# Kernel optimization log

Measured on AMD Instinct MI355X. Metric: run time of the kernel, lower is better.

Reference implementation:

```python
import jax, jax.numpy as jnp
from jax import lax
import numpy as np

K_IN, K_OUT, H, ML = 32, 16, 256, 80
L_PRE, L_FWD, B = 60, 80, 1024


def gru_cell(x, h, Wih, Whh, bih, bhh):
    # torch GRU gate order: r, z, n
    gi = x @ Wih.T + bih
    gh = h @ Whh.T + bhh
    ir, iz, inn = jnp.split(gi, 3, axis=-1)
    hr, hz, hn = jnp.split(gh, 3, axis=-1)
    r = jax.nn.sigmoid(ir + hr)
    z = jax.nn.sigmoid(iz + hz)
    n = jnp.tanh(inn + r * hn)
    return (1.0 - z) * n + z * h


def setup_inputs() -> dict:
    key = jax.random.key(0)
    ks = jax.random.split(key, 24)
    s = 0.05
    rn = lambda k, shp: (jax.random.normal(k, shp) * s).astype(jnp.float32)
    inp = {
        "pre_x": jax.random.normal(ks[0], (L_PRE, B, K_IN), dtype=jnp.float32),
        "pre_y": jax.random.normal(ks[1], (L_PRE, B, K_OUT), dtype=jnp.float32),
        "forward_x": jax.random.normal(ks[2], (L_FWD, B, K_IN), dtype=jnp.float32),
        # encoder: embedding Linear(k_in+k_out -> H), GRU(H,H)
        "enc_emb_W": rn(ks[3], (H, K_IN + K_OUT)),
        "enc_emb_b": rn(ks[4], (H,)),
        "enc_Wih": rn(ks[5], (3 * H, H)),
        "enc_Whh": rn(ks[6], (3 * H, H)),
        "enc_bih": rn(ks[7], (3 * H,)),
        "enc_bhh": rn(ks[8], (3 * H,)),
        # decoder: embedding Linear(k_out+k_in -> H), attn Linear(2H -> ML),
        # attn_combine Linear(2H -> H), GRU(H,H), out Linear(H -> k_out)
        "dec_emb_W": rn(ks[9], (H, K_OUT + K_IN)),
        "dec_emb_b": rn(ks[10], (H,)),
        "attn_W": rn(ks[11], (ML, 2 * H)),
        "attn_b": rn(ks[12], (ML,)),
        "comb_W": rn(ks[13], (H, 2 * H)),
        "comb_b": rn(ks[14], (H,)),
        "dec_Wih": rn(ks[15], (3 * H, H)),
        "dec_Whh": rn(ks[16], (3 * H, H)),
        "dec_bih": rn(ks[17], (3 * H,)),
        "dec_bhh": rn(ks[18], (3 * H,)),
        "out_W": rn(ks[19], (K_OUT, H)),
        "out_b": rn(ks[20], (K_OUT,)),
    }
    return inp


def reference(pre_x, pre_y, forward_x,
              enc_emb_W, enc_emb_b, enc_Wih, enc_Whh, enc_bih, enc_bhh,
              dec_emb_W, dec_emb_b, attn_W, attn_b, comb_W, comb_b,
              dec_Wih, dec_Whh, dec_bih, dec_bhh, out_W, out_b):
    L_pre, batch, _ = pre_x.shape
    hdim = enc_emb_b.shape[0]
    max_len = attn_b.shape[0]

    # ---- encoder ----
    emb = jnp.concatenate([pre_x, pre_y], axis=2) @ enc_emb_W.T + enc_emb_b  # [L_pre,B,H]
    h0 = jnp.zeros((batch, hdim), dtype=pre_x.dtype)

    def enc_step(h, x):
        h2 = gru_cell(x, h, enc_Wih, enc_Whh, enc_bih, enc_bhh)
        return h2, h2

    enc_h, enc_outs = lax.scan(enc_step, h0, emb)
    # pad encoder outputs to max_length along time (zeros beyond L_pre)
    enc_outputs = jnp.zeros((max_len, batch, hdim), dtype=pre_x.dtype).at[:L_pre].set(enc_outs)
    enc_bmh = enc_outputs.transpose(1, 0, 2)  # [B, ML, H]

    # ---- decoder (dropout inactive: eval mode) ----
    def dec_step(carry, fx):
        y, h = carry
        di = jnp.concatenate([y, fx], axis=-1)            # [B, k_out+k_in]
        e = di @ dec_emb_W.T + dec_emb_b                   # [B, H]
        logits = jnp.concatenate([e, h], axis=-1) @ attn_W.T + attn_b  # [B, ML]
        aw = jax.nn.softmax(logits, axis=-1)
        ctx = jnp.einsum('bm,bmh->bh', aw, enc_bmh)        # [B, H]
        g = jnp.tanh(jnp.concatenate([e, ctx], axis=-1) @ comb_W.T + comb_b)
        h2 = gru_cell(g, h, dec_Wih, dec_Whh, dec_bih, dec_bhh)
        y2 = h2 @ out_W.T + out_b                          # [B, k_out]
        return (y2, h2), y2

    y_init = jnp.zeros_like(pre_y[0])
    _, ys = lax.scan(dec_step, (y_init, enc_h), forward_x)
    return ys  # [L_fwd, B, k_out]
```

## Files before the change

### kernel.cpp

```cpp
#include <hip/hip_runtime.h>
#include <hip/hip_bf16.h>

#define BATCH 1024
#define HD 256
#define MLEN 80
#define LPRE 60
#define LFWD 80
#define KIN 32
#define KOUT 16

typedef unsigned short bf16_t;
typedef __attribute__((ext_vector_type(8))) short bf16x8;
typedef __attribute__((ext_vector_type(4))) float f32x4;
typedef __attribute__((ext_vector_type(4))) unsigned u32x4;

#define MFMA __builtin_amdgcn_mfma_f32_16x16x32_bf16

__device__ __forceinline__ float bf2f(bf16_t v){ return __uint_as_float(((unsigned)v)<<16); }
__device__ __forceinline__ bf16_t f2bf(float f){
    unsigned u = __float_as_uint(f);
    return (bf16_t)((u + 0x7FFFu + ((u>>16)&1u)) >> 16);
}
__device__ __forceinline__ unsigned pack2(float lo, float hi){
    return (unsigned)f2bf(lo) | ((unsigned)f2bf(hi)<<16);
}
__device__ __forceinline__ float bflo(unsigned d){ return __uint_as_float(d<<16); }
__device__ __forceinline__ float bfhi(unsigned d){ return __uint_as_float(d & 0xffff0000u); }
__device__ __forceinline__ float sigm(float x){ return 1.0f/(1.0f+__expf(-x)); }

#define OFF_Z  262144
#define OFF_IN 524288
#define OFF_HN 655360

__global__ void pack_gru(const float* __restrict__ Wih, const float* __restrict__ Whh,
                         bf16_t* __restrict__ dst)
{
    int T = blockIdx.x*256 + threadIdx.x;
    int grp, local;
    if (T < 16384){ grp=0; local=T; }
    else if (T < 32768){ grp=1; local=T-16384; }
    else if (T < 40960){ grp=2; local=T-32768; }
    else { grp=3; local=T-40960; }
    int nkt = (grp<2)?16:8;
    int nt  = local / (nkt*64);
    int rem = local - nt*(nkt*64);
    int kt  = rem >> 6;
    int l   = rem & 63;
    int n   = nt*16 + (l&15);
    int k0  = kt*32 + ((l>>4)<<3);
    unsigned w[4];
    #pragma unroll
    for (int h2=0; h2<4; h2++){
        float v[2];
        #pragma unroll
        for (int s=0; s<2; s++){
            int k = k0 + h2*2 + s;
            if (grp==0)      v[s] = (k<256)? Wih[(size_t)n*HD + k]       : Whh[(size_t)n*HD + (k-256)];
            else if (grp==1) v[s] = (k<256)? Wih[(size_t)(256+n)*HD + k] : Whh[(size_t)(256+n)*HD + (k-256)];
            else if (grp==2) v[s] = Wih[(size_t)(512+n)*HD + k];
            else             v[s] = Whh[(size_t)(512+n)*HD + k];
        }
        w[h2] = pack2(v[0], v[1]);
    }
    uint4 u = {w[0],w[1],w[2],w[3]};
    *(uint4*)((char*)dst + (size_t)T*16) = u;
}

__global__ void pack_B512(const float* __restrict__ W, bf16_t* __restrict__ dst)
{
    int T = blockIdx.x*256 + threadIdx.x;
    int nt = T >> 10, kt = (T>>6)&15, l = T&63;
    int n = nt*16 + (l&15);
    int k0 = kt*32 + ((l>>4)<<3);
    unsigned w[4];
    #pragma unroll
    for (int h2=0; h2<4; h2++)
        w[h2] = pack2(W[(size_t)n*512 + k0+h2*2], W[(size_t)n*512 + k0+h2*2+1]);
    uint4 u = {w[0],w[1],w[2],w[3]};
    *(uint4*)((char*)dst + (size_t)T*16) = u;
}

__global__ void wfuse_kernel(const float* __restrict__ dembW, const float* __restrict__ dembB,
                             const float* __restrict__ outW, const float* __restrict__ outB,
                             float* __restrict__ Wfuse, float* __restrict__ ebias)
{
    int T = blockIdx.x*256 + threadIdx.x;
    if (T < 65536){
        int k = T >> 8, n = T & 255;
        float acc = 0.f;
        #pragma unroll
        for (int o=0;o<16;o++) acc += dembW[(size_t)n*48 + o]*outW[(size_t)o*HD + k];
        Wfuse[(size_t)k*HD + n] = acc;
    } else if (T < 65792){
        int n = T - 65536;
        float acc = dembB[n];
        #pragma unroll
        for (int o=0;o<16;o++) acc += outB[o]*dembW[(size_t)n*48 + o];
        ebias[n] = acc;
    }
}

__global__ void pack_logits(const float* __restrict__ Wfuse, const float* __restrict__ dembW,
                            const float* __restrict__ attW, const float* __restrict__ attB,
                            const float* __restrict__ dembB, const float* __restrict__ ebias,
                            bf16_t* __restrict__ BL, bf16_t* __restrict__ BL0,
                            float* __restrict__ lb, float* __restrict__ lb0)
{
    int T = blockIdx.x*256 + threadIdx.x;
    if (T < 5760){
        int variant = (T < 2880) ? 0 : 1;
        int local = variant ? (T-2880) : T;
        int nt = local/576, rem = local - nt*576;
        int kt = rem >> 6, l = rem & 63;
        int m  = nt*16 + (l&15);
        int k0 = kt*32 + ((l>>4)<<3);
        unsigned w[4];
        #pragma unroll
        for (int h2=0; h2<4; h2++){
            float v[2];
            for (int s=0;s<2;s++){
                int k = k0 + h2*2 + s;
                float acc;
                if (kt < 8){
                    if (variant == 0){
                        acc = attW[(size_t)m*512 + 256 + k];
                        for (int n=0;n<256;n++) acc += Wfuse[(size_t)k*HD + n]*attW[(size_t)m*512 + n];
                    } else {
                        acc = attW[(size_t)m*512 + 256 + k];
                    }
                } else {
                    int kp = k - 256;
                    acc = 0.f;
                    for (int n=0;n<256;n++) acc += dembW[(size_t)n*48 + 16 + kp]*attW[(size_t)m*512 + n];
                }
                v[s] = acc;
            }
            w[h2] = pack2(v[0], v[1]);
        }
        uint4 u = {w[0],w[1],w[2],w[3]};
        bf16_t* d = variant ? BL0 : BL;
        *(uint4*)((char*)d + (size_t)local*16) = u;
    } else if (T < 5840){
        int m = T - 5760;
        float acc = attB[m];
        for (int n=0;n<256;n++) acc += ebias[n]*attW[(size_t)m*512 + n];
        lb[m] = acc;
    } else if (T < 5920){
        int m = T - 5840;
        float acc = attB[m];
        for (int n=0;n<256;n++) acc += dembB[n]*attW[(size_t)m*512 + n];
        lb0[m] = acc;
    }
}

__global__ void pack_gfold(const float* __restrict__ Wfuse, const float* __restrict__ dembW,
                           const float* __restrict__ combW, const float* __restrict__ combB,
                           const float* __restrict__ ebias, const float* __restrict__ dembB,
                           bf16_t* __restrict__ dst, float* __restrict__ cbf, float* __restrict__ cbf0)
{
    int T = blockIdx.x*256 + threadIdx.x;
    if (T < 9216){
        int nt = T/576, rem = T - nt*576;
        int kt = rem >> 6, l = rem & 63;
        int n = nt*16 + (l&15);
        int k0 = kt*32 + ((l>>4)<<3);
        unsigned w[4];
        for (int h2=0; h2<4; h2++){
            float v[2];
            for (int s=0;s<2;s++){
                int k = k0 + h2*2 + s;
                float acc = 0.f;
                if (k < 256){
                    for (int j=0;j<256;j++) acc += Wfuse[(size_t)k*HD + j]*combW[(size_t)n*512 + j];
                } else {
                    int kp = k - 256;
                    for (int j=0;j<256;j++) acc += dembW[(size_t)j*48 + 16 + kp]*combW[(size_t)n*512 + j];
                }
                v[s] = acc;
            }
            w[h2] = pack2(v[0], v[1]);
        }
        uint4 u = {w[0],w[1],w[2],w[3]};
        *(uint4*)((char*)dst + (size_t)T*16) = u;
    } else if (T < 9472){
        int n = T - 9216;
        float acc = combB[n];
        for (int j=0;j<256;j++) acc += ebias[j]*combW[(size_t)n*512 + j];
        cbf[n] = acc;
    } else if (T < 9728){
        int n = T - 9472;
        float acc = combB[n];
        for (int j=0;j<256;j++) acc += dembB[j]*combW[(size_t)n*512 + j];
        cbf0[n] = acc;
    }
}

__global__ void pack_out(const float* __restrict__ outW, bf16_t* __restrict__ dst)
{
    int T = blockIdx.x*256 + threadIdx.x;
    int kt = T >> 6, l = T & 63;
    int n  = l & 15;
    int k0 = kt*32 + ((l>>4)<<3);
    unsigned w[4];
    #pragma unroll
    for (int h2=0; h2<4; h2++)
        w[h2] = pack2(outW[(size_t)n*HD + k0+h2*2], outW[(size_t)n*HD + k0+h2*2+1]);
    uint4 u = {w[0],w[1],w[2],w[3]};
    *(uint4*)((char*)dst + (size_t)T*16) = u;
}

__global__ __launch_bounds__(256) void emb_kernel(
    const float* __restrict__ px, const float* __restrict__ py,
    const float* __restrict__ embW, const float* __restrict__ embB,
    bf16_t* __restrict__ emb)
{
    __shared__ float Ws[256*49];
    __shared__ float xy[16][48];
    __shared__ float bs[256];
    int t = blockIdx.y, b0 = blockIdx.x*16, tid = threadIdx.x;
    for (int i = tid; i < 256*48; i += 256){ int n=i/48, k=i-n*48; Ws[n*49+k]=embW[i]; }
    bs[tid] = embB[tid];
    for (int i = tid; i < 16*48; i += 256){
        int r=i/48, k=i-r*48;
        xy[r][k] = (k<KIN)? px[((size_t)t*BATCH + b0+r)*KIN + k]
                          : py[((size_t)t*BATCH + b0+r)*KOUT + (k-KIN)];
    }
    __syncthreads();
    int n = tid;
    const float* w = &Ws[n*49];
    for (int r=0;r<16;r++){
        float acc = bs[n];
        #pragma unroll
        for (int k=0;k<48;k++) acc += xy[r][k]*w[k];
        emb[((size_t)t*BATCH + b0+r)*HD + n] = f2bf(acc);
    }
}

__global__ void fxconv(const float* __restrict__ fx, bf16_t* __restrict__ dst)
{
    size_t i = (size_t)blockIdx.x*256 + threadIdx.x;
    const float4* s = (const float4*)(fx + i*8);
    float4 a = s[0], b = s[1];
    uint4 u = { pack2(a.x,a.y), pack2(a.z,a.w), pack2(b.x,b.y), pack2(b.z,b.w) };
    *(uint4*)(dst + i*8) = u;
}

__global__ __launch_bounds__(256) void pgemm(
    const bf16_t* __restrict__ enc, const bf16_t* __restrict__ Bcmb,
    bf16_t* __restrict__ P)
{
    __shared__ __align__(16) bf16_t As[16][264];
    __shared__ __align__(16) bf16_t Gs[16][264];
    int tid = threadIdx.x, b0 = blockIdx.x*16, t = blockIdx.y;
    const bf16_t* src = enc + ((size_t)t*BATCH + b0)*HD;
    for (int i = tid; i < 512; i += 256){
        int r = i>>5, c = i&31;
        *(uint4*)&As[r][c*8] = *(const uint4*)(src + (size_t)r*HD + c*8);
    }
    __syncthreads();
    int lane = tid&63, wave = tid>>6;
    const bf16_t* arow = &As[lane&15][(lane>>4)*8];
    size_t loff = (size_t)lane*16;
    #pragma unroll
    for (int u=0; u<4; u++){
        int nt = wave*4 + u;
        f32x4 c = {0,0,0,0};
        #pragma unroll
        for (int k8=0; k8<8; k8++){
            bf16x8 a = *(const bf16x8*)(arow + k8*32);
            bf16x8 b = *(const bf16x8*)((const char*)Bcmb + (size_t)(((nt<<4)+8+k8)<<10) + loff);
            c = MFMA(a, b, c, 0,0,0);
        }
        int n = (nt<<4) + (lane&15);
        #pragma unroll
        for (int q=0;q<4;q++) Gs[((lane>>4)<<2)+q][n] = f2bf(c[q]);
    }
    __syncthreads();
    bf16_t* dst = P + ((size_t)t*BATCH + b0)*HD;
    for (int i = tid; i < 512; i += 256){
        int r = i>>5, c = i&31;
        *(uint4*)(dst + (size_t)r*HD + c*8) = *(const uint4*)&Gs[r][c*8];
    }
}

__global__ __launch_bounds__(512) void gru_step2(
    const bf16_t* __restrict__ A0, const bf16_t* __restrict__ A1,
    const bf16_t* __restrict__ Bp,
    const float* __restrict__ bih, const float* __restrict__ bhh,
    const float* __restrict__ hprev, float* __restrict__ hnext,
    bf16_t* __restrict__ hnext_bf, bf16_t* __restrict__ extra_bf)
{
    __shared__ __align__(16) bf16_t As[16][520];
    __shared__ __align__(16) f32x4 redR[4][64];
    __shared__ __align__(16) f32x4 redZ[4][64];
    __shared__ __align__(16) f32x4 redI[4][64];
    int tid = threadIdx.x, b0 = blockIdx.x*16;
    for (int i = tid; i < 1024; i += 512){
        int r = i>>6, c = i&63;
        const bf16_t* src = (c<32)? (A0 + (size_t)(b0+r)*HD + c*8)
                                  : (A1 + (size_t)(b0+r)*HD + (c-32)*8);
        *(uint4*)&As[r][c*8] = *(const uint4*)src;
    }
    __syncthreads();
    int lane = tid & 63, wave = tid >> 6;
    int pairId = wave >> 1, half = wave & 1;
    int jt = blockIdx.y*4 + pairId;
    const char* arow = (const char*)&As[lane&15][(lane>>4)*8];
    const char* bpc = (const char*)Bp;
    size_t loff = (size_t)lane*16;
    size_t offX = half ? (size_t)OFF_HN : (size_t)OFF_IN;
    int kt0 = half*8;
    f32x4 cr={0,0,0,0}, cz={0,0,0,0}, cx={0,0,0,0};
    #pragma unroll
    for (int k8=0; k8<8; k8++){
        int kt = kt0 + k8;
        bf16x8 a  = *(const bf16x8*)(arow + kt*64);
        bf16x8 br = *(const bf16x8*)(bpc + (size_t)(((jt<<4)+kt)<<10) + loff);
        bf16x8 bz = *(const bf16x8*)(bpc + OFF_Z + (size_t)(((jt<<4)+kt)<<10) + loff);
        bf16x8 bx = *(const bf16x8*)(bpc + offX + (size_t)(((jt<<3)+k8)<<10) + loff);
        cr = MFMA(a, br, cr, 0,0,0);
        cz = MFMA(a, bz, cz, 0,0,0);
        cx = MFMA(a, bx, cx, 0,0,0);
    }
    if (half == 0){
        redR[pairId][lane] = cr;
        redZ[pairId][lane] = cz;
        redI[pairId][lane] = cx;
    }
    __syncthreads();
    if (half == 1){
        f32x4 crA = redR[pairId][lane];
        f32x4 czA = redZ[pairId][lane];
        f32x4 ci  = redI[pairId][lane];
        int j = (jt<<4) + (lane&15);
        float b_r = bih[j] + bhh[j];
        float b_z = bih[256+j] + bhh[256+j];
        float b_i = bih[512+j], b_h = bhh[512+j];
        #pragma unroll
        for (int q=0;q<4;q++){
            int b = b0 + ((lane>>4)<<2) + q;
            float rv = sigm(cr[q] + crA[q] + b_r);
            float zv = sigm(cz[q] + czA[q] + b_z);
            float nv = tanhf(ci[q] + b_i + rv*(cx[q] + b_h));
            float h2 = (1.0f - zv)*nv + zv*hprev[(size_t)b*HD + j];
            hnext[(size_t)b*HD + j] = h2;
            bf16_t hb = f2bf(h2);
            hnext_bf[(size_t)b*HD + j] = hb;
            extra_bf[(size_t)b*HD + j] = hb;
        }
    }
}

__global__ __launch_bounds__(512) void dec_attn(
    const bf16_t* __restrict__ hbf, const bf16_t* __restrict__ fxt,
    const bf16_t* __restrict__ BL, const bf16_t* __restrict__ Bout,
    const float* __restrict__ lbp, const float* __restrict__ outB,
    int t, float* __restrict__ aw, float* __restrict__ out)
{
    __shared__ __align__(16) bf16_t As[16][296];
    __shared__ float awL[16][84];
    int tid = threadIdx.x, b0 = blockIdx.x*16;
    for (int i = tid; i < 576; i += 512){
        int r = i/36, c = i - r*36;
        const bf16_t* src = (c<32)? (hbf + (size_t)(b0+r)*HD + c*8)
                                  : (fxt + (size_t)(b0+r)*KIN + (c-32)*8);
        *(uint4*)&As[r][c*8] = *(const uint4*)src;
    }
    __syncthreads();
    int lane = tid & 63, wave = tid >> 6;
    const bf16_t* arow = &As[lane&15][(lane>>4)*8];
    size_t loff = (size_t)lane*16;
    if (wave < 5){
        f32x4 c = {0,0,0,0};
        #pragma unroll
        for (int kt = 0; kt < 9; kt++){
            bf16x8 a = *(const bf16x8*)(arow + kt*32);
            bf16x8 b = *(const bf16x8*)((const char*)BL + (size_t)((wave*9+kt)<<10) + loff);
            c = MFMA(a, b, c, 0,0,0);
        }
        int m = (wave<<4) + (lane&15);
        float bbm = lbp[m];
        #pragma unroll
        for (int q=0;q<4;q++) awL[((lane>>4)<<2)+q][m] = c[q] + bbm;
    } else if (wave == 5 && t > 0){
        f32x4 c = {0,0,0,0};
        #pragma unroll
        for (int kt = 0; kt < 8; kt++){
            bf16x8 a = *(const bf16x8*)(arow + kt*32);
            bf16x8 b = *(const bf16x8*)((const char*)Bout + (size_t)(kt<<10) + loff);
            c = MFMA(a, b, c, 0,0,0);
        }
        int o = lane & 15;
        float bo = outB[o];
        #pragma unroll
        for (int q=0;q<4;q++){
            int r = ((lane>>4)<<2) + q;
            out[((size_t)(t-1)*BATCH + b0+r)*KOUT + o] = c[q] + bo;
        }
    }
    __syncthreads();
    if (tid < 256){
        int r2 = tid >> 4, l2 = tid & 15;
        float vmax = -1e30f;
        for (int m=l2; m<80; m+=16) vmax = fmaxf(vmax, awL[r2][m]);
        #pragma unroll
        for (int k=1; k<16; k<<=1) vmax = fmaxf(vmax, __shfl_xor(vmax, k, 16));
        float ps = 0.f;
        for (int m=l2; m<80; m+=16){ float v = __expf(awL[r2][m]-vmax); awL[r2][m]=v; ps += v; }
        #pragma unroll
        for (int k=1; k<16; k<<=1) ps += __shfl_xor(ps, k, 16);
        float inv = 1.0f/ps;
        for (int m=l2; m<80; m+=16) aw[(size_t)(b0+r2)*80 + m] = awL[r2][m]*inv;
    }
}

__global__ __launch_bounds__(256) void dec_gcomb(
    const bf16_t* __restrict__ hbf, const bf16_t* __restrict__ fxt,
    const float* __restrict__ aw, const bf16_t* __restrict__ P,
    const bf16_t* __restrict__ Bgf, const float* __restrict__ cbf,
    int kt0, bf16_t* __restrict__ g_out)
{
    __shared__ __align__(16) bf16_t As[16][296];
    __shared__ float aws[16][80];
    __shared__ float pre[16][68];
    __shared__ float part[2][16][64];
    int tid = threadIdx.x, b0 = blockIdx.x*16, y = blockIdx.y;

    int half = tid >> 7;
    int u = tid & 127;
    int r_ = u >> 3;
    int c8 = u & 7;
    const bf16_t* pbp = P + ((size_t)(half*30)*BATCH + (b0+r_))*HD + y*64 + c8*8;
    u32x4 pf[15];
    #pragma unroll
    for (int i=0;i<15;i++) pf[i] = *(const u32x4*)(pbp + (size_t)i*BATCH*HD);

    for (int i = tid; i < 576; i += 256){
        int r = i/36, c = i - r*36;
        const bf16_t* src = (c<32)? (hbf + (size_t)(b0+r)*HD + c*8)
                                  : (fxt + (size_t)(b0+r)*KIN + (c-32)*8);
        *(uint4*)&As[r][c*8] = *(const uint4*)src;
    }
    for (int i = tid; i < 1280; i += 256){
        int r = i/80, m = i - r*80;
        aws[r][m] = aw[(size_t)(b0+r)*80 + m];
    }
    __syncthreads();

    int lane = tid & 63, wave = tid >> 6;
    {
        const bf16_t* arow = &As[lane&15][(lane>>4)*8];
        size_t loff = (size_t)lane*16;
        int nt = y*4 + wave;
        f32x4 c = {0,0,0,0};
        for (int kt=kt0; kt<9; kt++){
            bf16x8 a = *(const bf16x8*)(arow + kt*32);
            bf16x8 b = *(const bf16x8*)((const char*)Bgf + (size_t)((nt*9+kt)<<10) + loff);
            c = MFMA(a, b, c, 0,0,0);
        }
        #pragma unroll
        for (int q=0;q<4;q++) pre[((lane>>4)<<2)+q][wave*16 + (lane&15)] = c[q];
    }

    float acc[8];
    #pragma unroll
    for (int i=0;i<8;i++) acc[i]=0.f;
    const float* awr = &aws[r_][half*30];
    #pragma unroll
    for (int i=0;i<15;i++){
        float w = awr[i];
        acc[0]=fmaf(w,bflo(pf[i][0]),acc[0]); acc[1]=fmaf(w,bfhi(pf[i][0]),acc[1]);
        acc[2]=fmaf(w,bflo(pf[i][1]),acc[2]); acc[3]=fmaf(w,bfhi(pf[i][1]),acc[3]);
        acc[4]=fmaf(w,bflo(pf[i][2]),acc[4]); acc[5]=fmaf(w,bfhi(pf[i][2]),acc[5]);
        acc[6]=fmaf(w,bflo(pf[i][3]),acc[6]); acc[7]=fmaf(w,bfhi(pf[i][3]),acc[7]);
    }
    #pragma unroll 5
    for (int i=15;i<30;i++){
        u32x4 v = *(const u32x4*)(pbp + (size_t)i*BATCH*HD);
        float w = awr[i];
        acc[0]=fmaf(w,bflo(v[0]),acc[0]); acc[1]=fmaf(w,bfhi(v[0]),acc[1]);
        acc[2]=fmaf(w,bflo(v[1]),acc[2]); acc[3]=fmaf(w,bfhi(v[1]),acc[3]);
        acc[4]=fmaf(w,bflo(v[2]),acc[4]); acc[5]=fmaf(w,bfhi(v[2]),acc[5]);
        acc[6]=fmaf(w,bflo(v[3]),acc[6]); acc[7]=fmaf(w,bfhi(v[3]),acc[7]);
    }
    {
        float4 p0 = {acc[0],acc[1],acc[2],acc[3]};
        float4 p1 = {acc[4],acc[5],acc[6],acc[7]};
        *(float4*)&part[half][r_][c8*8]   = p0;
        *(float4*)&part[half][r_][c8*8+4] = p1;
    }
    __syncthreads();

    if (tid < 128){
        int r = tid >> 3, cc = (tid & 7)*8;
        int n0 = y*64 + cc;
        unsigned ov[4];
        #pragma unroll
        for (int p2=0;p2<4;p2++){
            float g0 = tanhf(pre[r][cc+p2*2]   + part[0][r][cc+p2*2]   + part[1][r][cc+p2*2]   + cbf[n0+p2*2]);
            float g1 = tanhf(pre[r][cc+p2*2+1] + part[0][r][cc+p2*2+1] + part[1][r][cc+p2*2+1] + cbf[n0+p2*2+1]);
            ov[p2] = pack2(g0, g1);
        }
        uint4 uu = {ov[0],ov[1],ov[2],ov[3]};
        *(uint4*)(g_out + (size_t)(b0+r)*HD + n0) = uu;
    }
}

__global__ __launch_bounds__(256) void final79(
    const float* __restrict__ hf, const float* __restrict__ outW,
    const float* __restrict__ outB, float* __restrict__ ys)
{
    __shared__ float hs[16][260];
    __shared__ float ow[16*260];
    int tid = threadIdx.x, b0 = blockIdx.x*16;
    for (int i=tid;i<4096;i+=256){ int o2=i>>8,k=i&255; ow[o2*260+k]=outW[(size_t)o2*HD+k]; }
    for (int i=tid;i<4096;i+=256){ int r=i>>8,k=i&255; hs[r][k]=hf[(size_t)(b0+r)*HD+k]; }
    __syncthreads();
    int r=tid>>4, o=tid&15;
    float acc=outB[o];
    const float* w=&ow[o*260];
    for(int k=0;k<256;k++) acc += hs[r][k]*w[k];
    ys[((size_t)79*BATCH + b0+r)*KOUT + o] = acc;
}

extern "C" void kernel_launch(void* const* d_in, const int* in_sizes, int n_in,
                              void* d_out, int out_size, void* d_ws, size_t ws_size,
                              hipStream_t stream) {
    const float* pre_x    = (const float*)d_in[0];
    const float* pre_y    = (const float*)d_in[1];
    const float* fwd_x    = (const float*)d_in[2];
    const float* enc_embW = (const float*)d_in[3];
    const float* enc_embB = (const float*)d_in[4];
    const float* enc_Wih  = (const float*)d_in[5];
    const float* enc_Whh  = (const float*)d_in[6];
    const float* enc_bih  = (const float*)d_in[7];
    const float* enc_bhh  = (const float*)d_in[8];
    const float* dec_embW = (const float*)d_in[9];
    const float* dec_embB = (const float*)d_in[10];
    const float* attn_W   = (const float*)d_in[11];
    const float* attn_b   = (const float*)d_in[12];
    const float* comb_W   = (const float*)d_in[13];
    const float* comb_b   = (const float*)d_in[14];
    const float* dec_Wih  = (const float*)d_in[15];
    const float* dec_Whh  = (const float*)d_in[16];
    const float* dec_bih  = (const float*)d_in[17];
    const float* dec_bhh  = (const float*)d_in[18];
    const float* out_W    = (const float*)d_in[19];
    const float* out_b    = (const float*)d_in[20];
    float* out = (float*)d_out;

    char* ws = (char*)d_ws;
    size_t o = 0;
    auto alloc = [&](size_t bytes)->char*{
        char* p = ws + o; o = (o + bytes + 255) & ~(size_t)255; return p;
    };
    bf16_t* EMB     = (bf16_t*)alloc((size_t)LPRE*BATCH*HD*2);
    bf16_t* ENC_OUT = (bf16_t*)alloc((size_t)LPRE*BATCH*HD*2);
    bf16_t* PBUF    = (bf16_t*)alloc((size_t)LPRE*BATCH*HD*2);
    bf16_t* FXB     = (bf16_t*)alloc((size_t)LFWD*BATCH*KIN*2);
    float*  HF0     = (float*) alloc((size_t)BATCH*HD*4);
    float*  HF1     = (float*) alloc((size_t)BATCH*HD*4);
    bf16_t* HB0     = (bf16_t*)alloc((size_t)BATCH*HD*2);
    bf16_t* HB1     = (bf16_t*)alloc((size_t)BATCH*HD*2);
    bf16_t* GBUF    = (bf16_t*)alloc((size_t)BATCH*HD*2);
    bf16_t* DUMMY   = (bf16_t*)alloc((size_t)BATCH*HD*2);
    float*  AWB     = (float*) alloc((size_t)BATCH*80*4);
    float*  WFUSE   = (float*) alloc((size_t)256*256*4);
    float*  EBIAS   = (float*) alloc(256*4);
    float*  LB      = (float*) alloc(80*4);
    float*  LB0     = (float*) alloc(80*4);
    float*  CBF     = (float*) alloc(256*4);
    float*  CBF0    = (float*) alloc(256*4);
    bf16_t* PACK_ENC = (bf16_t*)alloc(786432);
    bf16_t* PACK_DEC = (bf16_t*)alloc(786432);
    bf16_t* PACK_CMB = (bf16_t*)alloc(262144);
    bf16_t* PACK_GF  = (bf16_t*)alloc(147456);
    bf16_t* PACK_BL  = (bf16_t*)alloc(46080);
    bf16_t* PACK_BL0 = (bf16_t*)alloc(46080);
    bf16_t* PACK_OUT = (bf16_t*)alloc(8192);

    hipMemsetAsync(HF0, 0, (size_t)BATCH*HD*4, stream);
    hipMemsetAsync(HB0, 0, (size_t)BATCH*HD*2, stream);

    dim3 blk(256);
    emb_kernel<<<dim3(64,60), blk, 0, stream>>>(pre_x, pre_y, enc_embW, enc_embB, EMB);
    fxconv<<<dim3(1280), blk, 0, stream>>>(fwd_x, FXB);
    pack_gru<<<dim3(192), blk, 0, stream>>>(enc_Wih, enc_Whh, PACK_ENC);
    pack_gru<<<dim3(192), blk, 0, stream>>>(dec_Wih, dec_Whh, PACK_DEC);
    pack_B512<<<dim3(64), blk, 0, stream>>>(comb_W, PACK_CMB);
    wfuse_kernel<<<dim3(257), blk, 0, stream>>>(dec_embW, dec_embB, out_W, out_b, WFUSE, EBIAS);
    pack_logits<<<dim3(24), blk, 0, stream>>>(WFUSE, dec_embW, attn_W, attn_b, dec_embB,
                                              EBIAS, PACK_BL, PACK_BL0, LB, LB0);
    pack_gfold<<<dim3(38), blk, 0, stream>>>(WFUSE, dec_embW, comb_W, comb_b,
                                             EBIAS, dec_embB, PACK_GF, CBF, CBF0);
    pack_out<<<dim3(2), blk, 0, stream>>>(out_W, PACK_OUT);

    float*  HF[2] = {HF0, HF1};
    bf16_t* HB[2] = {HB0, HB1};
    int p = 0;

    for (int t = 0; t < LPRE; t++){
        gru_step2<<<dim3(64,4), dim3(512), 0, stream>>>(
            EMB + (size_t)t*BATCH*HD, HB[p], PACK_ENC, enc_bih, enc_bhh,
            HF[p], HF[p^1], HB[p^1], ENC_OUT + (size_t)t*BATCH*HD);
        p ^= 1;
    }
    pgemm<<<dim3(64,60), blk, 0, stream>>>(ENC_OUT, PACK_CMB, PBUF);

    for (int t = 0; t < LFWD; t++){
        const bf16_t* fxt = FXB + (size_t)t*BATCH*KIN;
        dec_attn<<<dim3(64), dim3(512), 0, stream>>>(
            HB[p], fxt, t ? PACK_BL : PACK_BL0, PACK_OUT,
            t ? LB : LB0, out_b, t, AWB, out);
        dec_gcomb<<<dim3(64,4), blk, 0, stream>>>(
            HB[p], fxt, AWB, PBUF, PACK_GF, t ? CBF : CBF0, t ? 0 : 8, GBUF);
        gru_step2<<<dim3(64,4), dim3(512), 0, stream>>>(
            GBUF, HB[p], PACK_DEC, dec_bih, dec_bhh,
            HF[p], HF[p^1], HB[p^1], DUMMY);
        p ^= 1;
    }
    final79<<<dim3(64), blk, 0, stream>>>(HF[p], out_W, out_b, out);
}
```

Before: 2.553 ms.

## Fuse decoder attention and combine kernels into one 1024-thread block

Merges dec_attn and dec_gcomb into a single dec_front kernel, so the attention weights stay in shared memory instead of round-tripping through a global buffer, and one launch per decoder step is removed. Each block now handles all 256 hidden columns for 16 batch rows with 1024 threads, prefetching the P context rows while the attention logits are computed. The cost is fewer blocks (64 instead of 256 for the combine phase), heavier register and shared-memory use per block, and extra barriers, which may lower parallelism and latency hiding.

```diff
diff --git a/kernel.cpp b/kernel.cpp
--- a/kernel.cpp
+++ b/kernel.cpp
@@ -351,25 +351,45 @@
     }
 }
 
-__global__ __launch_bounds__(512) void dec_attn(
+__global__ __launch_bounds__(1024) void dec_front(
     const bf16_t* __restrict__ hbf, const bf16_t* __restrict__ fxt,
-    const bf16_t* __restrict__ BL, const bf16_t* __restrict__ Bout,
-    const float* __restrict__ lbp, const float* __restrict__ outB,
-    int t, float* __restrict__ aw, float* __restrict__ out)
+    const bf16_t* __restrict__ P,
+    const bf16_t* __restrict__ BL, const bf16_t* __restrict__ Bgf,
+    const bf16_t* __restrict__ Bout,
+    const float* __restrict__ lbp, const float* __restrict__ cbf,
+    const float* __restrict__ outB,
+    int t, bf16_t* __restrict__ g_out, float* __restrict__ out)
 {
     __shared__ __align__(16) bf16_t As[16][296];
     __shared__ float awL[16][84];
+    __shared__ float Cpart[16][256];
+    __shared__ float CbF[16][260];
+
     int tid = threadIdx.x, b0 = blockIdx.x*16;
-    for (int i = tid; i < 576; i += 512){
-        int r = i/36, c = i - r*36;
+
+    if (tid < 576){
+        int r = tid/36, c = tid - r*36;
         const bf16_t* src = (c<32)? (hbf + (size_t)(b0+r)*HD + c*8)
                                   : (fxt + (size_t)(b0+r)*KIN + (c-32)*8);
         *(uint4*)&As[r][c*8] = *(const uint4*)src;
     }
-    __syncthreads();
+
+    int half = tid >> 9;
+    int u    = tid & 511;
+    int cr_  = u >> 5;
+    int cc0  = (u & 31) * 8;
+    const bf16_t* cbp = P + ((size_t)(half*30)*BATCH + (b0+cr_))*HD + cc0;
+    u32x4 pf[10];
+    #pragma unroll
+    for (int i=0;i<10;i++) pf[i] = *(const u32x4*)(cbp + (size_t)i*BATCH*HD);
+
+    __syncthreads();
+
     int lane = tid & 63, wave = tid >> 6;
     const bf16_t* arow = &As[lane&15][(lane>>4)*8];
     size_t loff = (size_t)lane*16;
+    int kt0 = t ? 0 : 8;
+
     if (wave < 5){
         f32x4 c = {0,0,0,0};
         #pragma unroll
@@ -399,6 +419,7 @@
         }
     }
     __syncthreads();
+
     if (tid < 256){
         int r2 = tid >> 4, l2 = tid & 15;
         float vmax = -1e30f;
@@ -410,99 +431,65 @@
         #pragma unroll
         for (int k=1; k<16; k<<=1) ps += __shfl_xor(ps, k, 16);
         float inv = 1.0f/ps;
-        for (int m=l2; m<80; m+=16) aw[(size_t)(b0+r2)*80 + m] = awL[r2][m]*inv;
-    }
-}
-
-__global__ __launch_bounds__(256) void dec_gcomb(
-    const bf16_t* __restrict__ hbf, const bf16_t* __restrict__ fxt,
-    const float* __restrict__ aw, const bf16_t* __restrict__ P,
-    const bf16_t* __restrict__ Bgf, const float* __restrict__ cbf,
-    int kt0, bf16_t* __restrict__ g_out)
-{
-    __shared__ __align__(16) bf16_t As[16][296];
-    __shared__ float aws[16][80];
-    __shared__ float pre[16][68];
-    __shared__ float part[2][16][64];
-    int tid = threadIdx.x, b0 = blockIdx.x*16, y = blockIdx.y;
-
-    int half = tid >> 7;
-    int u = tid & 127;
-    int r_ = u >> 3;
-    int c8 = u & 7;
-    const bf16_t* pbp = P + ((size_t)(half*30)*BATCH + (b0+r_))*HD + y*64 + c8*8;
-    u32x4 pf[15];
+        for (int m=l2; m<80; m+=16) awL[r2][m] *= inv;
+    }
+    __syncthreads();
+
+    float acc[8];
     #pragma unroll
-    for (int i=0;i<15;i++) pf[i] = *(const u32x4*)(pbp + (size_t)i*BATCH*HD);
-
-    for (int i = tid; i < 576; i += 256){
-        int r = i/36, c = i - r*36;
-        const bf16_t* src = (c<32)? (hbf + (size_t)(b0+r)*HD + c*8)
-                                  : (fxt + (size_t)(b0+r)*KIN + (c-32)*8);
-        *(uint4*)&As[r][c*8] = *(const uint4*)src;
-    }
-    for (int i = tid; i < 1280; i += 256){
-        int r = i/80, m = i - r*80;
-        aws[r][m] = aw[(size_t)(b0+r)*80 + m];
-    }
-    __syncthreads();
-
-    int lane = tid & 63, wave = tid >> 6;
+    for (int i=0;i<8;i++) acc[i] = 0.f;
     {
-        const bf16_t* arow = &As[lane&15][(lane>>4)*8];
-        size_t loff = (size_t)lane*16;
-        int nt = y*4 + wave;
+        const float* awr = &awL[cr_][half*30];
+        #pragma unroll
+        for (int i=0;i<10;i++){
+            float w = awr[i];
+            acc[0]=fmaf(w,bflo(pf[i][0]),acc[0]); acc[1]=fmaf(w,bfhi(pf[i][0]),acc[1]);
+            acc[2]=fmaf(w,bflo(pf[i][1]),acc[2]); acc[3]=fmaf(w,bfhi(pf[i][1]),acc[3]);
+            acc[4]=fmaf(w,bflo(pf[i][2]),acc[4]); acc[5]=fmaf(w,bfhi(pf[i][2]),acc[5]);
+            acc[6]=fmaf(w,bflo(pf[i][3]),acc[6]); acc[7]=fmaf(w,bfhi(pf[i][3]),acc[7]);
+        }
+        #pragma unroll 5
+        for (int i=10;i<30;i++){
+            u32x4 v = *(const u32x4*)(cbp + (size_t)i*BATCH*HD);
+            float w = awr[i];
+            acc[0]=fmaf(w,bflo(v[0]),acc[0]); acc[1]=fmaf(w,bfhi(v[0]),acc[1]);
+            acc[2]=fmaf(w,bflo(v[1]),acc[2]); acc[3]=fmaf(w,bfhi(v[1]),acc[3]);
+            acc[4]=fmaf(w,bflo(v[2]),acc[4]); acc[5]=fmaf(w,bfhi(v[2]),acc[5]);
+            acc[6]=fmaf(w,bflo(v[3]),acc[6]); acc[7]=fmaf(w,bfhi(v[3]),acc[7]);
+        }
+    }
+    if (half == 0){
+        float4 p0 = {acc[0],acc[1],acc[2],acc[3]};
+        float4 p1 = {acc[4],acc[5],acc[6],acc[7]};
+        *(float4*)&Cpart[cr_][cc0]   = p0;
+        *(float4*)&Cpart[cr_][cc0+4] = p1;
+    }
+    __syncthreads();
+
+    if (half == 1){
+        float4 p0 = *(const float4*)&Cpart[cr_][cc0];
+        float4 p1 = *(const float4*)&Cpart[cr_][cc0+4];
+        float4 o0 = {acc[0]+p0.x, acc[1]+p0.y, acc[2]+p0.z, acc[3]+p0.w};
+        float4 o1 = {acc[4]+p1.x, acc[5]+p1.y, acc[6]+p1.z, acc[7]+p1.w};
+        *(float4*)&CbF[cr_][cc0]   = o0;
+        *(float4*)&CbF[cr_][cc0+4] = o1;
+    }
+    __syncthreads();
+
+    {
         f32x4 c = {0,0,0,0};
         for (int kt=kt0; kt<9; kt++){
             bf16x8 a = *(const bf16x8*)(arow + kt*32);
-            bf16x8 b = *(const bf16x8*)((const char*)Bgf + (size_t)((nt*9+kt)<<10) + loff);
+            bf16x8 b = *(const bf16x8*)((const char*)Bgf + (size_t)((wave*9+kt)<<10) + loff);
             c = MFMA(a, b, c, 0,0,0);
         }
-        #pragma unroll
-        for (int q=0;q<4;q++) pre[((lane>>4)<<2)+q][wave*16 + (lane&15)] = c[q];
-    }
-
-    float acc[8];
-    #pragma unroll
-    for (int i=0;i<8;i++) acc[i]=0.f;
-    const float* awr = &aws[r_][half*30];
-    #pragma unroll
-    for (int i=0;i<15;i++){
-        float w = awr[i];
-        acc[0]=fmaf(w,bflo(pf[i][0]),acc[0]); acc[1]=fmaf(w,bfhi(pf[i][0]),acc[1]);
-        acc[2]=fmaf(w,bflo(pf[i][1]),acc[2]); acc[3]=fmaf(w,bfhi(pf[i][1]),acc[3]);
-        acc[4]=fmaf(w,bflo(pf[i][2]),acc[4]); acc[5]=fmaf(w,bfhi(pf[i][2]),acc[5]);
-        acc[6]=fmaf(w,bflo(pf[i][3]),acc[6]); acc[7]=fmaf(w,bfhi(pf[i][3]),acc[7]);
-    }
-    #pragma unroll 5
-    for (int i=15;i<30;i++){
-        u32x4 v = *(const u32x4*)(pbp + (size_t)i*BATCH*HD);
-        float w = awr[i];
-        acc[0]=fmaf(w,bflo(v[0]),acc[0]); acc[1]=fmaf(w,bfhi(v[0]),acc[1]);
-        acc[2]=fmaf(w,bflo(v[1]),acc[2]); acc[3]=fmaf(w,bfhi(v[1]),acc[3]);
-        acc[4]=fmaf(w,bflo(v[2]),acc[4]); acc[5]=fmaf(w,bfhi(v[2]),acc[5]);
-        acc[6]=fmaf(w,bflo(v[3]),acc[6]); acc[7]=fmaf(w,bfhi(v[3]),acc[7]);
-    }
-    {
-        float4 p0 = {acc[0],acc[1],acc[2],acc[3]};
-        float4 p1 = {acc[4],acc[5],acc[6],acc[7]};
-        *(float4*)&part[half][r_][c8*8]   = p0;
-        *(float4*)&part[half][r_][c8*8+4] = p1;
-    }
-    __syncthreads();
-
-    if (tid < 128){
-        int r = tid >> 3, cc = (tid & 7)*8;
-        int n0 = y*64 + cc;
-        unsigned ov[4];
-        #pragma unroll
-        for (int p2=0;p2<4;p2++){
-            float g0 = tanhf(pre[r][cc+p2*2]   + part[0][r][cc+p2*2]   + part[1][r][cc+p2*2]   + cbf[n0+p2*2]);
-            float g1 = tanhf(pre[r][cc+p2*2+1] + part[0][r][cc+p2*2+1] + part[1][r][cc+p2*2+1] + cbf[n0+p2*2+1]);
-            ov[p2] = pack2(g0, g1);
-        }
-        uint4 uu = {ov[0],ov[1],ov[2],ov[3]};
-        *(uint4*)(g_out + (size_t)(b0+r)*HD + n0) = uu;
+        int n = (wave<<4) + (lane&15);
+        float bb = cbf[n];
+        #pragma unroll
+        for (int q=0;q<4;q++){
+            int r = ((lane>>4)<<2) + q;
+            g_out[(size_t)(b0+r)*HD + n] = f2bf(tanhf(c[q] + CbF[r][n] + bb));
+        }
     }
 }
 
@@ -564,7 +551,6 @@
     bf16_t* HB1     = (bf16_t*)alloc((size_t)BATCH*HD*2);
     bf16_t* GBUF    = (bf16_t*)alloc((size_t)BATCH*HD*2);
     bf16_t* DUMMY   = (bf16_t*)alloc((size_t)BATCH*HD*2);
-    float*  AWB     = (float*) alloc((size_t)BATCH*80*4);
     float*  WFUSE   = (float*) alloc((size_t)256*256*4);
     float*  EBIAS   = (float*) alloc(256*4);
     float*  LB      = (float*) alloc(80*4);
@@ -609,11 +595,11 @@
 
     for (int t = 0; t < LFWD; t++){
         const bf16_t* fxt = FXB + (size_t)t*BATCH*KIN;
-        dec_attn<<<dim3(64), dim3(512), 0, stream>>>(
-            HB[p], fxt, t ? PACK_BL : PACK_BL0, PACK_OUT,
-            t ? LB : LB0, out_b, t, AWB, out);
-        dec_gcomb<<<dim3(64,4), blk, 0, stream>>>(
-            HB[p], fxt, AWB, PBUF, PACK_GF, t ? CBF : CBF0, t ? 0 : 8, GBUF);
+        dec_front<<<dim3(64), dim3(1024), 0, stream>>>(
+            HB[p], fxt, PBUF,
+            t ? PACK_BL : PACK_BL0, PACK_GF, PACK_OUT,
+            t ? LB : LB0, t ? CBF : CBF0, out_b,
+            t, GBUF, out);
         gru_step2<<<dim3(64,4), dim3(512), 0, stream>>>(
             GBUF, HB[p], PACK_DEC, dec_bih, dec_bhh,
             HF[p], HF[p^1], HB[p^1], DUMMY);
```

New measurement: 2.391 ms. -6.3%, faster.
